# Optimization experiments

Hardware: AMD Instinct MI355X
Metric: run time of the kernel (lower is better)

The kernel has to match this reference:

```python
import jax, jax.numpy as jnp
import numpy as np

B, T, V, E, D = 64, 512, 512, 128, 256


def setup_inputs() -> dict:
    key = jax.random.key(0)
    ks = jax.random.split(key, 9)
    g = lambda k, sh, s: jax.random.normal(k, sh, jnp.float32) * np.float32(s)
    return {
        "x": jax.random.randint(ks[0], (B, T), 0, V),
        "embed": g(ks[1], (V, E), 1.0),
        "W_ih": g(ks[2], (E, D), 1.0 / np.sqrt(E)),
        "W_hh": g(ks[3], (D, D), 1.0 / np.sqrt(D)),
        "b_h": jnp.zeros((D,), jnp.float32),
        "W_attn": g(ks[4], (D, D), 1.0 / np.sqrt(D)),
        "U_attn": g(ks[5], (D, D), 1.0 / np.sqrt(D)),
        "v_attn": g(ks[6], (D,), 1.0 / np.sqrt(D)),
        "fc_W": g(ks[7], (2 * D, V), 1.0 / np.sqrt(2 * D)),
        "fc_b": jnp.zeros((V,), jnp.float32),
    }


def _forward(x, embed, W_ih, W_hh, b_h, W_attn, U_attn, v_attn, fc_W, fc_b):
    Bn, Tn = x.shape
    Dn = W_hh.shape[0]
    # precompute input projection for every step: [T, B, D]
    xp = jnp.swapaxes(embed[x] @ W_ih + b_h, 0, 1)
    pos = jnp.arange(Tn)

    def step(carry, x_t):
        h_prev, Hbuf, Pbuf, t = carry  # Hbuf: past hidden states, Pbuf: W_attn-projected
        h = jnp.tanh(x_t + h_prev @ W_hh)  # [B, D]
        # Bahdanau attention over strictly-past states (slots < t)
        cur_proj = h @ U_attn  # [B, D]
        energy = jnp.einsum('tbd,d->tb', jnp.tanh(Pbuf + cur_proj[None]), v_attn)
        energy = jnp.where((pos < t)[:, None], energy, -1e9)
        w = jax.nn.softmax(energy, axis=0)  # [T, B]
        ctx = jnp.einsum('tb,tbd->bd', w, Hbuf)
        ctx = jnp.where(t == 0, h, ctx)  # first step: context = h itself
        logits = jnp.concatenate([h, ctx], axis=-1) @ fc_W + fc_b  # [B, V]
        Hbuf = Hbuf.at[t].set(h)
        Pbuf = Pbuf.at[t].set(h @ W_attn)
        return (h, Hbuf, Pbuf, t + 1), logits

    h0 = jnp.zeros((Bn, Dn), xp.dtype)
    buf = jnp.zeros((Tn, Bn, Dn), xp.dtype)
    _, outs = jax.lax.scan(step, (h0, buf, buf, jnp.asarray(0, jnp.int32)), xp)
    return jnp.swapaxes(outs, 0, 1)  # [B, T, V]


def reference(x, embed, W_ih, W_hh, b_h, W_attn, U_attn, v_attn, fc_W, fc_b):
    return _forward(x, embed, W_ih, W_hh, b_h, W_attn, U_attn, v_attn, fc_W, fc_b)
```

## Files before the change

kernel.cpp:

```cpp
#include <hip/hip_runtime.h>
#include <hip/hip_bf16.h>

#define B_  64
#define T_  512
#define V_  512
#define E_  128
#define D_  256
#define D2_ 512

typedef unsigned short u16;
typedef unsigned int   u32;
typedef short s16x8 __attribute__((ext_vector_type(8)));
typedef _Float16 f16x8 __attribute__((ext_vector_type(8)));
typedef float f32x4 __attribute__((ext_vector_type(4)));
typedef unsigned short u16x2 __attribute__((ext_vector_type(2)));
typedef unsigned short u16x4 __attribute__((ext_vector_type(4)));

__device__ __forceinline__ float bf2f(u16 u){
    union { u32 i; float f; } c; c.i = ((u32)u) << 16; return c.f;
}
__device__ __forceinline__ u16 f2bf(float f){
    union { float f; u32 i; } c; c.f = f;
    u32 u = c.i;
    return (u16)((u + 0x7fffu + ((u >> 16) & 1u)) >> 16);
}
__device__ __forceinline__ u16 f2h(float f){
    union { _Float16 h; u16 u; } c; c.h = (_Float16)f; return c.u;
}
__device__ __forceinline__ float tanh_b(float x){
    float e = __expf(2.0f * x);
    return fmaf(-2.0f, __builtin_amdgcn_rcpf(e + 1.0f), 1.0f);
}
__device__ __forceinline__ void barrier_lgkm(){
    asm volatile("s_waitcnt lgkmcnt(0)\n\ts_barrier" ::: "memory");
}

__global__ __launch_bounds__(256) void k_ew(const float* __restrict__ embed,
                                            const float* __restrict__ W_ih,
                                            const float* __restrict__ b_h,
                                            float* __restrict__ EW){
    __shared__ float er[E_];
    int v = blockIdx.x;
    int tid = threadIdx.x;
    if (tid < E_) er[tid] = embed[v*E_ + tid];
    __syncthreads();
    float acc = b_h[tid];
    #pragma unroll 4
    for (int e = 0; e < E_; ++e) acc += er[e] * W_ih[e*D_ + tid];
    EW[v*D_ + tid] = acc;
}

__global__ __launch_bounds__(256) void k_gather(const int* __restrict__ x,
                                                const float* __restrict__ EW,
                                                float* __restrict__ XP){
    int m = blockIdx.x * 4 + (threadIdx.x >> 6);
    int lane = threadIdx.x & 63;
    int b = m & 63, t = m >> 6;
    int v = x[b*T_ + t];
    float4 val = *(const float4*)&EW[v*D_ + lane*4];
    *(float4*)&XP[(size_t)m*D_ + lane*4] = val;
}

__global__ __launch_bounds__(256) void k_cvt(const float* __restrict__ W,
                                             u16* __restrict__ Wb,
                                             int N, int K){
    int i = blockIdx.x * 256 + threadIdx.x;
    int n = i / K, k = i - n*K;
    Wb[(size_t)n*K + k] = f2bf(W[(size_t)k*N + n]);
}

__global__ __launch_bounds__(512, 2) void k_rnn(const float* __restrict__ XP,
                                                const float* __restrict__ W_hh,
                                                u16* __restrict__ HC){
    __shared__ u16 hf[2][4][272];
    int tid  = threadIdx.x;
    int lane = tid & 63;
    int w    = tid >> 6;
    int col  = lane & 15;
    int colA = col & 3;
    int quad = lane >> 4;
    int bb0  = blockIdx.x * 4;

    f16x8 bfh[2][8];
    #pragma unroll
    for (int nt = 0; nt < 2; ++nt){
        int n = w*32 + nt*16 + col;
        #pragma unroll
        for (int ks = 0; ks < 8; ++ks){
            f16x8 th;
            #pragma unroll
            for (int j = 0; j < 8; ++j){
                int k = ks*32 + quad*8 + j;
                th[j] = (_Float16)W_hh[k*D_ + n];
            }
            bfh[nt][ks] = th;
        }
    }
    for (int i = tid; i < 2*4*272; i += 512) (&hf[0][0][0])[i] = 0;

    const float* p  = XP + (size_t)bb0*D_ + w*32 + col;
    u16*         hc = HC + (size_t)bb0*D2_ + w*32 + col;

    float ewv[2][4];
    #pragma unroll
    for (int nt = 0; nt < 2; ++nt)
        #pragma unroll
        for (int r = 0; r < 4; ++r)
            ewv[nt][r] = p[r*D_ + nt*16];
    p += (size_t)B_*D_;
    __syncthreads();

    for (int t = 0; t < T_; ++t){
        int rb = t & 1, wb = rb ^ 1;
        f32x4 acc[2];
        #pragma unroll
        for (int nt = 0; nt < 2; ++nt)
            #pragma unroll
            for (int r = 0; r < 4; ++r) acc[nt][r] = ewv[nt][r];

        f16x8 ah[8];
        #pragma unroll
        for (int ks = 0; ks < 8; ++ks)
            ah[ks] = *(const f16x8*)&hf[rb][colA][ks*32 + quad*8];

        if (t + 1 < T_){
            #pragma unroll
            for (int nt = 0; nt < 2; ++nt)
                #pragma unroll
                for (int r = 0; r < 4; ++r)
                    ewv[nt][r] = p[r*D_ + nt*16];
        }
        p += (size_t)B_*D_;

        #pragma unroll
        for (int ks = 0; ks < 8; ++ks){
            acc[0] = __builtin_amdgcn_mfma_f32_16x16x32_f16(ah[ks], bfh[0][ks], acc[0], 0, 0, 0);
            acc[1] = __builtin_amdgcn_mfma_f32_16x16x32_f16(ah[ks], bfh[1][ks], acc[1], 0, 0, 0);
        }

        #pragma unroll
        for (int nt = 0; nt < 2; ++nt){
            f32x4 s = acc[nt];
            float v = (quad & 2) ? ((quad & 1) ? s[3] : s[2])
                                 : ((quad & 1) ? s[1] : s[0]);
            float h  = tanh_b(v);
            int n    = w*32 + nt*16 + col;
            hf[wb][quad][n]      = f2h(h);
            hc[quad*D2_ + nt*16] = f2bf(h);
        }
        hc += (size_t)B_*D2_;
        barrier_lgkm();
    }
}

__global__ __launch_bounds__(256) void k_gemm(const u16* __restrict__ A, int lda,
                                              const u16* __restrict__ Wb,
                                              const float* __restrict__ bias,
                                              void* __restrict__ out,
                                              int K, int N, int mode){
    __shared__ u16 As[64][88];
    __shared__ u16 Ws[64][88];
    int tid  = threadIdx.x;
    int lane = tid & 63;
    int w    = tid >> 6;
    int col  = lane & 15;
    int quad = lane >> 4;
    int m0   = blockIdx.x * 64;
    int n0   = blockIdx.y * 64;

    f32x4 acc[4];
    #pragma unroll
    for (int nt = 0; nt < 4; ++nt)
        #pragma unroll
        for (int r = 0; r < 4; ++r) acc[nt][r] = 0.0f;

    for (int kk = 0; kk < K; kk += 64){
        #pragma unroll
        for (int i = 0; i < 2; ++i){
            int idx = tid + i*256;
            int r   = idx >> 3;
            int c8  = (idx & 7) * 8;
            *(s16x8*)&As[r][c8] = *(const s16x8*)&A [(size_t)(m0 + r)*lda + kk + c8];
            *(s16x8*)&Ws[r][c8] = *(const s16x8*)&Wb[(size_t)(n0 + r)*K   + kk + c8];
        }
        barrier_lgkm();
        #pragma unroll
        for (int ks = 0; ks < 2; ++ks){
            s16x8 a = *(const s16x8*)&As[w*16 + col][ks*32 + quad*8];
            #pragma unroll
            for (int nt = 0; nt < 4; ++nt){
                s16x8 b = *(const s16x8*)&Ws[nt*16 + col][ks*32 + quad*8];
                acc[nt] = __builtin_amdgcn_mfma_f32_16x16x32_bf16(a, b, acc[nt], 0, 0, 0);
            }
        }
        barrier_lgkm();
    }
    #pragma unroll
    for (int nt = 0; nt < 4; ++nt){
        int n = n0 + nt*16 + col;
        float bv = (mode == 1 && bias) ? bias[n] : 0.0f;
        #pragma unroll
        for (int r = 0; r < 4; ++r){
            int m = m0 + w*16 + quad*4 + r;
            float v = acc[nt][r] + bv;
            if (mode == 1){
                int b = m & 63, t = m >> 6;
                ((float*)out)[(size_t)(b*T_ + t)*V_ + n] = v;
            } else if (mode == 2){
                ((u16*)out)[(size_t)m*N + n] = f2bf(__expf(2.0f * v));
            } else if (mode == 3){
                u16* dst = (u16*)out + ((size_t)(n >> 8)) * ((size_t)32768 * 256);
                dst[(size_t)m*256 + (n & 255)] = f2bf(__expf(2.0f * v));
            } else {
                ((u16*)out)[(size_t)m*N + n] = f2bf(v);
            }
        }
    }
}

__global__ __launch_bounds__(512) void k_fc(const u16* __restrict__ A,
                                            const u16* __restrict__ Wb,
                                            const float* __restrict__ bias,
                                            float* __restrict__ out){
    __shared__ u16 As[128][88];
    __shared__ u16 Ws[128][88];
    int tid  = threadIdx.x;
    int lane = tid & 63;
    int w    = tid >> 6;
    int wm   = w >> 2;
    int wn   = w & 3;
    int col  = lane & 15;
    int quad = lane >> 4;
    int m0   = blockIdx.x * 128;
    int n0   = blockIdx.y * 128;

    f32x4 acc[4][2];
    #pragma unroll
    for (int mt = 0; mt < 4; ++mt)
        #pragma unroll
        for (int nt = 0; nt < 2; ++nt)
            #pragma unroll
            for (int r = 0; r < 4; ++r) acc[mt][nt][r] = 0.0f;

    for (int kk = 0; kk < D2_; kk += 64){
        #pragma unroll
        for (int i = 0; i < 2; ++i){
            int idx = tid + i*512;
            int r   = idx >> 3;
            int c8  = (idx & 7) * 8;
            *(s16x8*)&As[r][c8] = *(const s16x8*)&A [(size_t)(m0 + r)*D2_ + kk + c8];
            *(s16x8*)&Ws[r][c8] = *(const s16x8*)&Wb[(size_t)(n0 + r)*D2_ + kk + c8];
        }
        barrier_lgkm();
        #pragma unroll
        for (int ks = 0; ks < 2; ++ks){
            s16x8 b0 = *(const s16x8*)&Ws[wn*32 +      col][ks*32 + quad*8];
            s16x8 b1 = *(const s16x8*)&Ws[wn*32 + 16 + col][ks*32 + quad*8];
            #pragma unroll
            for (int mt = 0; mt < 4; ++mt){
                s16x8 a = *(const s16x8*)&As[wm*64 + mt*16 + col][ks*32 + quad*8];
                acc[mt][0] = __builtin_amdgcn_mfma_f32_16x16x32_bf16(a, b0, acc[mt][0], 0, 0, 0);
                acc[mt][1] = __builtin_amdgcn_mfma_f32_16x16x32_bf16(a, b1, acc[mt][1], 0, 0, 0);
            }
        }
        barrier_lgkm();
    }
    #pragma unroll
    for (int nt = 0; nt < 2; ++nt){
        int n = n0 + wn*32 + nt*16 + col;
        float bv = bias[n];
        #pragma unroll
        for (int mt = 0; mt < 4; ++mt){
            #pragma unroll
            for (int r = 0; r < 4; ++r){
                int m = m0 + wm*64 + mt*16 + quad*4 + r;
                int b = m & 63, t = m >> 6;
                out[(size_t)(b*T_ + t)*V_ + n] = acc[mt][nt][r] + bv;
            }
        }
    }
}

__global__ __launch_bounds__(256) void k_energy(const u16* __restrict__ EP,
                                                const u16* __restrict__ EQ,
                                                const float* __restrict__ v_attn,
                                                u16* __restrict__ Wx,
                                                float* __restrict__ l){
    __shared__ float eps[32][288];
    int tid = threadIdx.x;
    int blk = blockIdx.x;
    int b   = blk / 136;
    int pi  = blk % 136;
    int tt  = 0;
    while ((tt+1)*(tt+2)/2 <= pi) ++tt;
    int pt  = pi - tt*(tt+1)/2;

    int t_l = tid >> 3;
    int dg  = tid & 7;
    int d0  = dg * 32;
    int t   = tt*32 + t_l;

    #pragma unroll
    for (int i = 0; i < 8; ++i){
        int idx = tid + i*256;
        int row = idx >> 6;
        int c4  = (idx & 63) * 4;
        int pc  = c4 + ((c4 >> 5) << 2);
        u16x4 v4 = *(const u16x4*)&EP[((size_t)((pt*32 + row)*B_ + b))*D_ + c4];
        float4 f4 = make_float4(bf2f(v4.x), bf2f(v4.y), bf2f(v4.z), bf2f(v4.w));
        *(float4*)&eps[row][pc] = f4;
    }

    float eq[32], vm2[32], sv = 0.0f;
    #pragma unroll
    for (int i = 0; i < 8; ++i){
        u16x4 v4 = *(const u16x4*)&EQ[((size_t)(t*B_ + b))*D_ + d0 + i*4];
        eq[i*4+0] = bf2f(v4.x); eq[i*4+1] = bf2f(v4.y);
        eq[i*4+2] = bf2f(v4.z); eq[i*4+3] = bf2f(v4.w);
    }
    #pragma unroll
    for (int i = 0; i < 32; ++i){
        float v = v_attn[d0 + i];
        sv += v;
        vm2[i] = -2.0f * v;
    }
    barrier_lgkm();

    float lsum = 0.0f;
    for (int tpl = 0; tpl < 32; ++tpl){
        int tp = pt*32 + tpl;
        float acc = sv;
        #pragma unroll
        for (int g = 0; g < 8; ++g){
            float4 ep = *(const float4*)&eps[tpl][dg*36 + 4*g];
            float da = fmaf(ep.x, eq[4*g+0], 1.0f);
            float db = fmaf(ep.y, eq[4*g+1], 1.0f);
            float dc = fmaf(ep.z, eq[4*g+2], 1.0f);
            float dd = fmaf(ep.w, eq[4*g+3], 1.0f);
            float dab = da * db;
            float dcd = dc * dd;
            float nab = fmaf(vm2[4*g+1], da, vm2[4*g+0] * db);
            float ncd = fmaf(vm2[4*g+3], dc, vm2[4*g+2] * dd);
            float num = fmaf(ncd, dab, nab * dcd);
            acc = fmaf(num, __builtin_amdgcn_rcpf(dab * dcd), acc);
        }
        acc += __shfl_xor(acc, 1);
        acc += __shfl_xor(acc, 2);
        acc += __shfl_xor(acc, 4);
        float pe = __expf(acc);
        if (dg == 0 && tp < t){
            u16 peb = f2bf(pe);
            Wx[((size_t)(b*T_ + t))*T_ + tp] = peb;
            lsum += bf2f(peb);
        }
    }
    if (dg == 0 && lsum != 0.0f) atomicAdd(&l[b*T_ + t], lsum);
}

__global__ __launch_bounds__(256) void k_ctx(const u16* __restrict__ Wx,
                                             u16* __restrict__ HC,
                                             const float* __restrict__ l){
    __shared__ u16 As[64][88];
    __shared__ u16 Ws[64][88];
    int tid  = threadIdx.x;
    int lane = tid & 63;
    int w    = tid >> 6;
    int col  = lane & 15;
    int quad = lane >> 4;
    int b    = blockIdx.y;
    int m0   = (blockIdx.x >> 2) * 64;
    int n0   = (blockIdx.x & 3) * 64;

    const u16* A = Wx + (size_t)b * T_ * T_;

    f32x4 acc[4];
    #pragma unroll
    for (int nt = 0; nt < 4; ++nt)
        #pragma unroll
        for (int r = 0; r < 4; ++r) acc[nt][r] = 0.0f;

    int kmax = m0 + 64;
    for (int kk = 0; kk < kmax; kk += 64){
        #pragma unroll
        for (int i = 0; i < 2; ++i){
            int idx = tid + i*256;
            int r   = idx >> 3;
            int c8  = (idx & 7) * 8;
            *(s16x8*)&As[r][c8] = *(const s16x8*)&A[(size_t)(m0 + r)*T_ + kk + c8];
        }
        #pragma unroll
        for (int i = 0; i < 8; ++i){
            int idx = tid + i*256;
            int k   = idx >> 5;
            int n2  = (idx & 31) * 2;
            u16x2 v2 = *(const u16x2*)&HC[((size_t)((kk + k)*B_ + b))*D2_ + n0 + n2];
            Ws[n2][k]   = v2.x;
            Ws[n2+1][k] = v2.y;
        }
        barrier_lgkm();
        #pragma unroll
        for (int ks = 0; ks < 2; ++ks){
            s16x8 a = *(const s16x8*)&As[w*16 + col][ks*32 + quad*8];
            #pragma unroll
            for (int nt = 0; nt < 4; ++nt){
                s16x8 bb = *(const s16x8*)&Ws[nt*16 + col][ks*32 + quad*8];
                acc[nt] = __builtin_amdgcn_mfma_f32_16x16x32_bf16(a, bb, acc[nt], 0, 0, 0);
            }
        }
        barrier_lgkm();
    }

    float linv[4];
    #pragma unroll
    for (int r = 0; r < 4; ++r){
        int t = m0 + w*16 + quad*4 + r;
        float lv = (t > 0) ? l[b*T_ + t] : 1.0f;
        linv[r] = 1.0f / lv;
    }
    #pragma unroll
    for (int nt = 0; nt < 4; ++nt){
        int n = n0 + nt*16 + col;
        #pragma unroll
        for (int r = 0; r < 4; ++r){
            int t = m0 + w*16 + quad*4 + r;
            u16 ov;
            if (t == 0) ov = HC[(size_t)b*D2_ + n];
            else        ov = f2bf(acc[nt][r] * linv[r]);
            HC[((size_t)(t*B_ + b))*D2_ + D_ + n] = ov;
        }
    }
}

extern "C" void kernel_launch(void* const* d_in, const int* in_sizes, int n_in,
                              void* d_out, int out_size, void* d_ws, size_t ws_size,
                              hipStream_t stream){
    const int*   x     = (const int*)d_in[0];
    const float* embed = (const float*)d_in[1];
    const float* W_ih  = (const float*)d_in[2];
    const float* W_hh  = (const float*)d_in[3];
    const float* b_h   = (const float*)d_in[4];
    const float* W_att = (const float*)d_in[5];
    const float* U_att = (const float*)d_in[6];
    const float* v_att = (const float*)d_in[7];
    const float* fc_W  = (const float*)d_in[8];
    const float* fc_b  = (const float*)d_in[9];

    char* ws = (char*)d_ws;
    float* EW   = (float*)ws;
    u16*   fcWb = (u16*)ws;
    u16*   HC   = (u16*)(ws + 524288);
    u16*   EP   = (u16*)(ws + 34078720);
    u16*   EQ   = (u16*)(ws + 50855936);
    float* XP   = (float*)(ws + 34078720);
    float* l    = (float*)(ws + 67633152);
    u16*   Wab  = (u16*)(ws + 67764224);
    u16*   Uab  = (u16*)(ws + 67895296);
    u16*   Wx   = (u16*)d_out;

    (void)hipMemsetAsync(d_out, 0, (size_t)B_*T_*T_*2, stream);
    (void)hipMemsetAsync(l, 0, B_*T_*4, stream);

    k_ew    <<<dim3(V_),          dim3(256), 0, stream>>>(embed, W_ih, b_h, EW);
    k_gather<<<dim3(T_*B_/4),     dim3(256), 0, stream>>>(x, EW, XP);
    k_cvt   <<<dim3(D_*D_/256),   dim3(256), 0, stream>>>(W_att, Wab, D_, D_);
    k_cvt   <<<dim3(D_*D_/256),   dim3(256), 0, stream>>>(U_att, Uab, D_, D_);
    k_cvt   <<<dim3(D2_*V_/256),  dim3(256), 0, stream>>>(fc_W, fcWb, V_, D2_);
    k_rnn   <<<dim3(16),          dim3(512), 0, stream>>>(XP, W_hh, HC);
    k_gemm  <<<dim3(512, 8),      dim3(256), 0, stream>>>(HC, D2_, Wab, nullptr, (void*)EP, D_, D2_, 3);
    k_energy<<<dim3(B_*136),      dim3(256), 0, stream>>>(EP, EQ, v_att, Wx, l);
    k_ctx   <<<dim3(32, B_),      dim3(256), 0, stream>>>(Wx, HC, l);
    k_fc    <<<dim3(256, 4),      dim3(512), 0, stream>>>(HC, fcWb, fc_b, (float*)d_out);
}
```

Baseline: 702.7 us.

## Fuse prep kernels, gather embeddings inside RNN, drop memsets and atomics

Merges the embedding projection and three weight conversion kernels into one launch. The RNN now reads token ids and looks up the projected embedding rows directly, so the XP gather buffer and its kernel go away. The two memsets and the atomic row-sum are removed: k_ctx masks the diagonal tile itself and computes the softmax denominators from the tiles it already loads. This trades redundant launches and global traffic for more scattered loads inside the latency-bound serial RNN loop.

```diff
diff --git a/kernel.cpp b/kernel.cpp
--- a/kernel.cpp
+++ b/kernel.cpp
@@ -35,41 +35,45 @@
     asm volatile("s_waitcnt lgkmcnt(0)\n\ts_barrier" ::: "memory");
 }
 
-__global__ __launch_bounds__(256) void k_ew(const float* __restrict__ embed,
-                                            const float* __restrict__ W_ih,
-                                            const float* __restrict__ b_h,
-                                            float* __restrict__ EW){
+__global__ __launch_bounds__(256) void k_ew_cvt(const float* __restrict__ embed,
+                                                const float* __restrict__ W_ih,
+                                                const float* __restrict__ b_h,
+                                                float* __restrict__ EW,
+                                                const float* __restrict__ W_att,
+                                                const float* __restrict__ U_att,
+                                                const float* __restrict__ fc_W,
+                                                u16* __restrict__ Wab,
+                                                u16* __restrict__ Uab,
+                                                u16* __restrict__ fcWb){
     __shared__ float er[E_];
-    int v = blockIdx.x;
+    int blk = blockIdx.x;
     int tid = threadIdx.x;
-    if (tid < E_) er[tid] = embed[v*E_ + tid];
-    __syncthreads();
-    float acc = b_h[tid];
-    #pragma unroll 4
-    for (int e = 0; e < E_; ++e) acc += er[e] * W_ih[e*D_ + tid];
-    EW[v*D_ + tid] = acc;
-}
-
-__global__ __launch_bounds__(256) void k_gather(const int* __restrict__ x,
+    if (blk < V_){
+        if (tid < E_) er[tid] = embed[blk*E_ + tid];
+        __syncthreads();
+        float acc = b_h[tid];
+        #pragma unroll 4
+        for (int e = 0; e < E_; ++e) acc += er[e] * W_ih[e*D_ + tid];
+        EW[blk*D_ + tid] = acc;
+    } else {
+        int i = (blk - V_) * 256 + tid;
+        if (i < 65536){
+            int n = i >> 8, k = i & 255;
+            Wab[i] = f2bf(W_att[k*D_ + n]);
+        } else if (i < 131072){
+            int j = i - 65536;
+            int n = j >> 8, k = j & 255;
+            Uab[j] = f2bf(U_att[k*D_ + n]);
+        } else {
+            int j = i - 131072;
+            int n = j >> 9, k = j & 511;
+            fcWb[j] = f2bf(fc_W[k*V_ + n]);
+        }
+    }
+}
+
+__global__ __launch_bounds__(512, 2) void k_rnn(const int* __restrict__ x,
                                                 const float* __restrict__ EW,
-                                                float* __restrict__ XP){
-    int m = blockIdx.x * 4 + (threadIdx.x >> 6);
-    int lane = threadIdx.x & 63;
-    int b = m & 63, t = m >> 6;
-    int v = x[b*T_ + t];
-    float4 val = *(const float4*)&EW[v*D_ + lane*4];
-    *(float4*)&XP[(size_t)m*D_ + lane*4] = val;
-}
-
-__global__ __launch_bounds__(256) void k_cvt(const float* __restrict__ W,
-                                             u16* __restrict__ Wb,
-                                             int N, int K){
-    int i = blockIdx.x * 256 + threadIdx.x;
-    int n = i / K, k = i - n*K;
-    Wb[(size_t)n*K + k] = f2bf(W[(size_t)k*N + n]);
-}
-
-__global__ __launch_bounds__(512, 2) void k_rnn(const float* __restrict__ XP,
                                                 const float* __restrict__ W_hh,
                                                 u16* __restrict__ HC){
     __shared__ u16 hf[2][4][272];
@@ -80,6 +84,7 @@
     int colA = col & 3;
     int quad = lane >> 4;
     int bb0  = blockIdx.x * 4;
+    int dofs = w*32 + col;
 
     f16x8 bfh[2][8];
     #pragma unroll
@@ -98,16 +103,22 @@
     }
     for (int i = tid; i < 2*4*272; i += 512) (&hf[0][0][0])[i] = 0;
 
-    const float* p  = XP + (size_t)bb0*D_ + w*32 + col;
-    u16*         hc = HC + (size_t)bb0*D2_ + w*32 + col;
-
+    u16* hc = HC + (size_t)bb0*D2_ + w*32 + col;
+
+    int vnext[4];
     float ewv[2][4];
-    #pragma unroll
-    for (int nt = 0; nt < 2; ++nt)
-        #pragma unroll
-        for (int r = 0; r < 4; ++r)
-            ewv[nt][r] = p[r*D_ + nt*16];
-    p += (size_t)B_*D_;
+    {
+        int vcur[4];
+        #pragma unroll
+        for (int r = 0; r < 4; ++r) vcur[r]  = x[(bb0 + r)*T_ + 0];
+        #pragma unroll
+        for (int r = 0; r < 4; ++r) vnext[r] = x[(bb0 + r)*T_ + 1];
+        #pragma unroll
+        for (int nt = 0; nt < 2; ++nt)
+            #pragma unroll
+            for (int r = 0; r < 4; ++r)
+                ewv[nt][r] = EW[vcur[r]*D_ + dofs + nt*16];
+    }
     __syncthreads();
 
     for (int t = 0; t < T_; ++t){
@@ -128,9 +139,12 @@
             for (int nt = 0; nt < 2; ++nt)
                 #pragma unroll
                 for (int r = 0; r < 4; ++r)
-                    ewv[nt][r] = p[r*D_ + nt*16];
-        }
-        p += (size_t)B_*D_;
+                    ewv[nt][r] = EW[vnext[r]*D_ + dofs + nt*16];
+        }
+        if (t + 2 < T_){
+            #pragma unroll
+            for (int r = 0; r < 4; ++r) vnext[r] = x[(bb0 + r)*T_ + t + 2];
+        }
 
         #pragma unroll
         for (int ks = 0; ks < 8; ++ks){
@@ -284,8 +298,7 @@
 __global__ __launch_bounds__(256) void k_energy(const u16* __restrict__ EP,
                                                 const u16* __restrict__ EQ,
                                                 const float* __restrict__ v_attn,
-                                                u16* __restrict__ Wx,
-                                                float* __restrict__ l){
+                                                u16* __restrict__ Wx){
     __shared__ float eps[32][288];
     int tid = threadIdx.x;
     int blk = blockIdx.x;
@@ -326,7 +339,6 @@
     }
     barrier_lgkm();
 
-    float lsum = 0.0f;
     for (int tpl = 0; tpl < 32; ++tpl){
         int tp = pt*32 + tpl;
         float acc = sv;
@@ -347,21 +359,17 @@
         acc += __shfl_xor(acc, 1);
         acc += __shfl_xor(acc, 2);
         acc += __shfl_xor(acc, 4);
-        float pe = __expf(acc);
         if (dg == 0 && tp < t){
-            u16 peb = f2bf(pe);
-            Wx[((size_t)(b*T_ + t))*T_ + tp] = peb;
-            lsum += bf2f(peb);
-        }
-    }
-    if (dg == 0 && lsum != 0.0f) atomicAdd(&l[b*T_ + t], lsum);
+            Wx[((size_t)(b*T_ + t))*T_ + tp] = f2bf(__expf(acc));
+        }
+    }
 }
 
 __global__ __launch_bounds__(256) void k_ctx(const u16* __restrict__ Wx,
-                                             u16* __restrict__ HC,
-                                             const float* __restrict__ l){
+                                             u16* __restrict__ HC){
     __shared__ u16 As[64][88];
     __shared__ u16 Ws[64][88];
+    __shared__ float rs[64];
     int tid  = threadIdx.x;
     int lane = tid & 63;
     int w    = tid >> 6;
@@ -373,6 +381,10 @@
 
     const u16* A = Wx + (size_t)b * T_ * T_;
 
+    int r0 = tid >> 3;
+    int c8 = (tid & 7) * 8;
+    float rsum0 = 0.0f, rsum1 = 0.0f;
+
     f32x4 acc[4];
     #pragma unroll
     for (int nt = 0; nt < 4; ++nt)
@@ -381,12 +393,21 @@
 
     int kmax = m0 + 64;
     for (int kk = 0; kk < kmax; kk += 64){
+        bool diag = (kk == m0);
         #pragma unroll
         for (int i = 0; i < 2; ++i){
-            int idx = tid + i*256;
-            int r   = idx >> 3;
-            int c8  = (idx & 7) * 8;
-            *(s16x8*)&As[r][c8] = *(const s16x8*)&A[(size_t)(m0 + r)*T_ + kk + c8];
+            int r = r0 + i*32;
+            s16x8 v = *(const s16x8*)&A[(size_t)(m0 + r)*T_ + kk + c8];
+            if (diag){
+                #pragma unroll
+                for (int j = 0; j < 8; ++j)
+                    if (c8 + j >= r) v[j] = 0;
+            }
+            *(s16x8*)&As[r][c8] = v;
+            float s = 0.0f;
+            #pragma unroll
+            for (int j = 0; j < 8; ++j) s += bf2f((u16)v[j]);
+            if (i == 0) rsum0 += s; else rsum1 += s;
         }
         #pragma unroll
         for (int i = 0; i < 8; ++i){
@@ -410,11 +431,16 @@
         barrier_lgkm();
     }
 
+    rsum0 += __shfl_xor(rsum0, 1); rsum0 += __shfl_xor(rsum0, 2); rsum0 += __shfl_xor(rsum0, 4);
+    rsum1 += __shfl_xor(rsum1, 1); rsum1 += __shfl_xor(rsum1, 2); rsum1 += __shfl_xor(rsum1, 4);
+    if ((tid & 7) == 0){ rs[r0] = rsum0; rs[r0 + 32] = rsum1; }
+    barrier_lgkm();
+
     float linv[4];
     #pragma unroll
     for (int r = 0; r < 4; ++r){
-        int t = m0 + w*16 + quad*4 + r;
-        float lv = (t > 0) ? l[b*T_ + t] : 1.0f;
+        int rr = w*16 + quad*4 + r;
+        float lv = (m0 + rr > 0) ? rs[rr] : 1.0f;
         linv[r] = 1.0f / lv;
     }
     #pragma unroll
@@ -447,27 +473,20 @@
 
     char* ws = (char*)d_ws;
     float* EW   = (float*)ws;
-    u16*   fcWb = (u16*)ws;
-    u16*   HC   = (u16*)(ws + 524288);
-    u16*   EP   = (u16*)(ws + 34078720);
-    u16*   EQ   = (u16*)(ws + 50855936);
-    float* XP   = (float*)(ws + 34078720);
-    float* l    = (float*)(ws + 67633152);
-    u16*   Wab  = (u16*)(ws + 67764224);
-    u16*   Uab  = (u16*)(ws + 67895296);
+    u16*   Wab  = (u16*)(ws + 524288);
+    u16*   Uab  = (u16*)(ws + 655360);
+    u16*   fcWb = (u16*)(ws + 786432);
+    u16*   HC   = (u16*)(ws + 1310720);
+    u16*   EP   = (u16*)(ws + 34865152);
+    u16*   EQ   = (u16*)(ws + 51642368);
     u16*   Wx   = (u16*)d_out;
 
-    (void)hipMemsetAsync(d_out, 0, (size_t)B_*T_*T_*2, stream);
-    (void)hipMemsetAsync(l, 0, B_*T_*4, stream);
-
-    k_ew    <<<dim3(V_),          dim3(256), 0, stream>>>(embed, W_ih, b_h, EW);
-    k_gather<<<dim3(T_*B_/4),     dim3(256), 0, stream>>>(x, EW, XP);
-    k_cvt   <<<dim3(D_*D_/256),   dim3(256), 0, stream>>>(W_att, Wab, D_, D_);
-    k_cvt   <<<dim3(D_*D_/256),   dim3(256), 0, stream>>>(U_att, Uab, D_, D_);
-    k_cvt   <<<dim3(D2_*V_/256),  dim3(256), 0, stream>>>(fc_W, fcWb, V_, D2_);
-    k_rnn   <<<dim3(16),          dim3(512), 0, stream>>>(XP, W_hh, HC);
+    k_ew_cvt<<<dim3(2048),        dim3(256), 0, stream>>>(embed, W_ih, b_h, EW,
+                                                          W_att, U_att, fc_W,
+                                                          Wab, Uab, fcWb);
+    k_rnn   <<<dim3(16),          dim3(512), 0, stream>>>(x, EW, W_hh, HC);
     k_gemm  <<<dim3(512, 8),      dim3(256), 0, stream>>>(HC, D2_, Wab, nullptr, (void*)EP, D_, D2_, 3);
-    k_energy<<<dim3(B_*136),      dim3(256), 0, stream>>>(EP, EQ, v_att, Wx, l);
-    k_ctx   <<<dim3(32, B_),      dim3(256), 0, stream>>>(Wx, HC, l);
+    k_energy<<<dim3(B_*136),      dim3(256), 0, stream>>>(EP, EQ, v_att, Wx);
+    k_ctx   <<<dim3(32, B_),      dim3(256), 0, stream>>>(Wx, HC);
     k_fc    <<<dim3(256, 4),      dim3(512), 0, stream>>>(HC, fcWb, fc_b, (float*)d_out);
 }
```

After: 713.4 us. No clear change (+1.5%).
